# Kernel optimization log

Measured on AMD Instinct MI355X. Metric: run time of the kernel, lower is better.

The kernel has to match this reference:

```python
import jax, jax.numpy as jnp
import numpy as np

QK_DIM = 1024
V_DIM = 1024
NUM_HEADS = 16
HEAD_DIM = 64
INNER = NUM_HEADS * HEAD_DIM  # 1024
SCALE = HEAD_DIM ** -0.5


def setup_inputs() -> dict:
    key = jax.random.key(0)
    ks = jax.random.split(key, 8)
    m, nq, nkv = 4, 2048, 2048
    xq = jax.random.normal(ks[0], (m, nq, QK_DIM), dtype=jnp.float32)
    xk = jax.random.normal(ks[1], (m, nkv, QK_DIM), dtype=jnp.float32)
    xv = jax.random.normal(ks[2], (m, nkv, V_DIM), dtype=jnp.float32)
    # torch nn.Linear weights are [out, in]; y = x @ W.T
    s_qk = (QK_DIM) ** -0.5
    s_in = (INNER) ** -0.5
    Wq = jax.random.uniform(ks[3], (INNER, QK_DIM), jnp.float32, -s_qk, s_qk)
    Wk = jax.random.uniform(ks[4], (INNER, QK_DIM), jnp.float32, -s_qk, s_qk)
    Wv = jax.random.uniform(ks[5], (INNER, V_DIM), jnp.float32, -s_qk, s_qk)
    Wo = jax.random.uniform(ks[6], (V_DIM, INNER), jnp.float32, -s_in, s_in)
    bo = jax.random.uniform(ks[7], (V_DIM,), jnp.float32, -s_in, s_in)
    return {"xq": xq, "xk": xk, "xv": xv, "Wq": Wq, "Wk": Wk, "Wv": Wv, "Wo": Wo, "bo": bo}


def reference(xq, xk, xv, Wq, Wk, Wv, Wo, bo):
    m, nq, _ = xq.shape
    nkv = xk.shape[1]
    # projections (no bias), split heads: b n (h d) -> b h n d
    q = (xq @ Wq.T).reshape(m, nq, NUM_HEADS, HEAD_DIM).transpose(0, 2, 1, 3)
    k = (xk @ Wk.T).reshape(m, nkv, NUM_HEADS, HEAD_DIM).transpose(0, 2, 1, 3)
    v = (xv @ Wv.T).reshape(m, nkv, NUM_HEADS, HEAD_DIM).transpose(0, 2, 1, 3)
    dots = jnp.einsum("bhqd,bhkd->bhqk", q, k) * SCALE  # [m,h,nq,nkv]
    attn = jax.nn.softmax(dots, axis=-1)
    out = jnp.einsum("bhqk,bhkd->bhqd", attn, v)
    out = out.transpose(0, 2, 1, 3).reshape(m, nq, INNER)  # b h n d -> b n (h d)
    return out @ Wo.T + bo  # to_out Linear (dropout p=0 -> identity)
```

## Files before the change

### kernel.cpp

```cpp
#include <hip/hip_runtime.h>

typedef unsigned short u16;
using bf16x8 = __attribute__((ext_vector_type(8))) __bf16;
using f32x4  = __attribute__((ext_vector_type(4))) float;

#define QSCALE 0.18033688011f

#define EXP2F(x) __builtin_amdgcn_exp2f(x)
#define SCHED_FENCE() __builtin_amdgcn_sched_barrier(0)

__device__ __forceinline__ u16 f2bf(float f) {
  union { float f; unsigned int u; } x; x.f = f;
  unsigned int r = x.u + 0x7FFFu + ((x.u >> 16) & 1u);
  return (u16)(r >> 16);
}

__device__ __forceinline__ bf16x8 ld8(const u16* p) {
  return *reinterpret_cast<const bf16x8*>(p);
}

__device__ __forceinline__ void gload16(const void* g, void* l) {
  __builtin_amdgcn_global_load_lds(
      (const __attribute__((address_space(1))) unsigned int*)g,
      (__attribute__((address_space(3))) unsigned int*)l, 16, 0, 0);
}

__device__ __forceinline__ void cast8(const float* __restrict__ src, u16* __restrict__ dst,
                                      size_t i8) {
  const float4 v0 = reinterpret_cast<const float4*>(src)[i8 * 2];
  const float4 v1 = reinterpret_cast<const float4*>(src)[i8 * 2 + 1];
  ushort4 o0, o1;
  o0.x = f2bf(v0.x); o0.y = f2bf(v0.y); o0.z = f2bf(v0.z); o0.w = f2bf(v0.w);
  o1.x = f2bf(v1.x); o1.y = f2bf(v1.y); o1.z = f2bf(v1.z); o1.w = f2bf(v1.w);
  uint4 o;
  o.x = (unsigned)o0.x | ((unsigned)o0.y << 16);
  o.y = (unsigned)o0.z | ((unsigned)o0.w << 16);
  o.z = (unsigned)o1.x | ((unsigned)o1.y << 16);
  o.w = (unsigned)o1.z | ((unsigned)o1.w << 16);
  reinterpret_cast<uint4*>(dst)[i8] = o;
}

__global__ void cast3_f32_to_bf16(const float* __restrict__ a, const float* __restrict__ b,
                                  const float* __restrict__ c, u16* __restrict__ out, int n8) {
  const int y = blockIdx.y;
  const float* src = (y == 0) ? a : (y == 1) ? b : c;
  u16* dst = out + (size_t)y * n8 * 8;
  const int stride = gridDim.x * 256;
  for (size_t i = blockIdx.x * 256 + threadIdx.x; i < (size_t)n8; i += stride)
    cast8(src, dst, i);
}

__global__ void cast4_f32_to_bf16(const float* __restrict__ a, const float* __restrict__ b,
                                  const float* __restrict__ c, const float* __restrict__ d,
                                  u16* __restrict__ out, int n8) {
  const int y = blockIdx.y;
  const float* src = (y == 0) ? a : (y == 1) ? b : (y == 2) ? c : d;
  u16* dst = out + (size_t)y * n8 * 8;
  const int stride = gridDim.x * 256;
  for (size_t i = blockIdx.x * 256 + threadIdx.x; i < (size_t)n8; i += stride)
    cast8(src, dst, i);
}

#define GEMM64_BODY(A_, B_)                                                          \
  __shared__ alignas(16) u16 lds_a[2][128 * 64];                                     \
  __shared__ alignas(16) u16 lds_b[2][128 * 64];                                     \
  const int t = threadIdx.x;                                                         \
  const int w = t >> 6, lane = t & 63;                                               \
  const int wr = w >> 1, wc = w & 1;                                                 \
  f32x4 acc[4][4];                                                                   \
  _Pragma("unroll") for (int i = 0; i < 4; ++i)                                      \
    _Pragma("unroll") for (int j = 0; j < 4; ++j) acc[i][j] = {0.f, 0.f, 0.f, 0.f};  \
  const int b_r = t >> 3;                                                            \
  const int b_c = ((t & 7) ^ (b_r & 7)) * 8;                                         \
  const u16* gaa = A_ + (row0 + b_r) * 1024 + b_c;                                   \
  const u16* gbb = B_ + (col0 + b_r) * 1024 + b_c;                                   \
  const int fr = lane & 15;                                                          \
  const int flh = lane >> 4;                                                         \
  const int fx7 = fr & 7;                                                            \
  _Pragma("unroll") for (int s = 0; s < 4; ++s) {                                    \
    gload16(gaa + (size_t)(32 * s) * 1024, &lds_a[0][s * 2048 + w * 512]);           \
    gload16(gbb + (size_t)(32 * s) * 1024, &lds_b[0][s * 2048 + w * 512]);           \
  }                                                                                  \
  for (int it = 0; it < 16; ++it) {                                                  \
    const int cur = it & 1;                                                          \
    asm volatile("s_waitcnt vmcnt(0)" ::: "memory");                                 \
    SCHED_FENCE();                                                                   \
    __syncthreads();                                                                 \
    SCHED_FENCE();                                                                   \
    if (it != 15) {                                                                  \
      const int nk = (it + 1) * 64;                                                  \
      _Pragma("unroll") for (int s = 0; s < 4; ++s) {                                \
        gload16(gaa + (size_t)(32 * s) * 1024 + nk, &lds_a[cur ^ 1][s * 2048 + w * 512]); \
        gload16(gbb + (size_t)(32 * s) * 1024 + nk, &lds_b[cur ^ 1][s * 2048 + w * 512]); \
      }                                                                              \
    }                                                                                \
    SCHED_FENCE();                                                                   \
    _Pragma("unroll") for (int ks2 = 0; ks2 < 2; ++ks2) {                            \
      bf16x8 af[4], bfr[4];                                                          \
      const int gch = ks2 * 4 + flh;                                                 \
      _Pragma("unroll") for (int i = 0; i < 4; ++i)                                  \
        af[i] = ld8(&lds_a[cur][(wr * 64 + i * 16 + fr) * 64 + ((gch ^ fx7) * 8)]);  \
      _Pragma("unroll") for (int j = 0; j < 4; ++j)                                  \
        bfr[j] = ld8(&lds_b[cur][(wc * 64 + j * 16 + fr) * 64 + ((gch ^ fx7) * 8)]); \
      _Pragma("unroll") for (int i = 0; i < 4; ++i)                                  \
        _Pragma("unroll") for (int j = 0; j < 4; ++j)                                \
          acc[i][j] = __builtin_amdgcn_mfma_f32_16x16x32_bf16(af[i], bfr[j], acc[i][j], 0, 0, 0); \
    }                                                                                \
  }                                                                                  \
  const int er = (lane >> 4) * 4, ec = lane & 15;

__global__ __launch_bounds__(256)
void gemm_qkv(const u16* __restrict__ Aall, const u16* __restrict__ Ball,
              u16* __restrict__ Call) {
  const int g = (blockIdx.x & 7) * 192 + (blockIdx.x >> 3);
  const int bx = g & 7, by = (g >> 3) & 63, z = g >> 9;
  const u16* A = Aall + (size_t)z * 8192 * 1024;
  const u16* B = Ball + (size_t)z * 1024 * 1024;
  u16* C = Call + (size_t)z * 8192 * 1024;
  const size_t row0 = (size_t)by * 128;
  const size_t col0 = (size_t)bx * 128;

  GEMM64_BODY(A, B)

#pragma unroll
  for (int i = 0; i < 4; ++i)
#pragma unroll
    for (int j = 0; j < 4; ++j) {
      const size_t row = row0 + wr * 64 + i * 16 + er;
      const size_t col = col0 + wc * 64 + j * 16 + ec;
      if (z == 0) {
#pragma unroll
        for (int r = 0; r < 4; ++r)
          C[(row + r) * 1024 + col] = f2bf(acc[i][j][r] * QSCALE);
      } else if (z == 1) {
#pragma unroll
        for (int r = 0; r < 4; ++r) {
          const size_t n = row + r;
          const size_t colswz = (col & ~(size_t)63) |
                                ((col & 63) ^ (((n & 7) << 3)));
          C[n * 1024 + colswz] = f2bf(acc[i][j][r]);
        }
      } else {
        ushort4 o4;
        o4.x = f2bf(acc[i][j][0]); o4.y = f2bf(acc[i][j][1]);
        o4.z = f2bf(acc[i][j][2]); o4.w = f2bf(acc[i][j][3]);
        const size_t nloc = row & 2047;
        const size_t d = col & 63;
        size_t pos = (nloc & ~(size_t)31) | (((nloc >> 2) & 3) << 3) |
                     (((nloc >> 4) & 1) << 2) | (nloc & 3);
        pos ^= (d & 7) << 3;
        const size_t idx = (((row >> 11) * 16 + (col >> 6)) * 64 + d) * 2048 + pos;
        *reinterpret_cast<ushort4*>(&C[idx]) = o4;
      }
    }
}

__global__ __launch_bounds__(256)
void gemm_out(const u16* __restrict__ A, const u16* __restrict__ B,
              float* __restrict__ Cf, const float* __restrict__ bias) {
  const int g = (blockIdx.x & 7) * 64 + (blockIdx.x >> 3);
  const int bx = g & 7, by = g >> 3;
  const size_t row0 = (size_t)by * 128;
  const size_t col0 = (size_t)bx * 128;

  GEMM64_BODY(A, B)

#pragma unroll
  for (int i = 0; i < 4; ++i)
#pragma unroll
    for (int j = 0; j < 4; ++j) {
      const size_t row = row0 + wr * 64 + i * 16 + er;
      const size_t col = col0 + wc * 64 + j * 16 + ec;
#pragma unroll
      for (int r = 0; r < 4; ++r)
        Cf[(row + r) * 1024 + col] = acc[i][j][r] + bias[col];
    }
}

__global__ __launch_bounds__(512)
void flash_attn(const u16* __restrict__ Q, const u16* __restrict__ Km,
                const u16* __restrict__ Vt, u16* __restrict__ O) {
  const int o_blk = (blockIdx.x & 7) * 64 + (blockIdx.x >> 3);
  const int qt = o_blk & 7, h = (o_blk >> 3) & 15, b = o_blk >> 7;
  const int t = threadIdx.x;
  const int w = t >> 6, lane = t & 63;
  const int l16 = lane & 15, lh = lane >> 4;

  __shared__ alignas(16) u16 kt_lds[2][64][64];
  __shared__ alignas(16) u16 vt_lds[2][64][64];

  const size_t base_qk = ((size_t)b * 2048) * 1024 + (size_t)h * 64;
  const size_t base_vt = ((size_t)(b * 16 + h)) * 64 * 2048;

  bf16x8 qf[2][2];
#pragma unroll
  for (int g = 0; g < 2; ++g) {
    const size_t qrow = (size_t)qt * 256 + (w * 2 + g) * 16 + l16;
    const u16* qp = Q + base_qk + qrow * 1024 + lh * 8;
    qf[g][0] = ld8(qp);
    qf[g][1] = ld8(qp + 32);
  }

  bf16x8 vones;
#pragma unroll
  for (int i = 0; i < 8; ++i) vones[i] = (__bf16)1.0f;

  f32x4 o_acc[2][4];
  f32x4 o_sum[2];
#pragma unroll
  for (int g = 0; g < 2; ++g) {
#pragma unroll
    for (int j = 0; j < 4; ++j) o_acc[g][j] = {0.f, 0.f, 0.f, 0.f};
    o_sum[g] = {0.f, 0.f, 0.f, 0.f};
  }

  const int srow = t >> 3;
  const int schk = (t & 7) * 8;
  const u16* kg = Km + base_qk + (size_t)srow * 1024 + schk;
  const u16* vg = Vt + base_vt + (size_t)srow * 2048 + schk;
  u16* kl0 = &kt_lds[0][0][0] + w * 512;
  u16* kl1 = &kt_lds[1][0][0] + w * 512;
  u16* vl0 = &vt_lds[0][0][0] + w * 512;
  u16* vl1 = &vt_lds[1][0][0] + w * 512;

  gload16(kg, kl0);
  gload16(vg, vl0);

  const int xo = (l16 & 7) << 3;

  for (int it = 0; it < 32; ++it) {
    const int cur = it & 1;
    asm volatile("s_waitcnt vmcnt(0)" ::: "memory");
    SCHED_FENCE();
    __syncthreads();
    SCHED_FENCE();

    if (it != 31) {
      const int nkv = (it + 1) * 64;
      gload16(kg + (size_t)nkv * 1024, cur ? kl0 : kl1);
      gload16(vg + nkv, cur ? vl0 : vl1);
    }
    SCHED_FENCE();

    f32x4 s[2][4];
#pragma unroll
    for (int g = 0; g < 2; ++g)
#pragma unroll
      for (int j = 0; j < 4; ++j) s[g][j] = {0.f, 0.f, 0.f, 0.f};
    __builtin_amdgcn_s_setprio(1);
#pragma unroll
    for (int j = 0; j < 4; ++j)
#pragma unroll
      for (int ks = 0; ks < 2; ++ks) {
        bf16x8 kf = ld8(&kt_lds[cur][j * 16 + l16][(ks * 32 + lh * 8) ^ xo]);
        s[0][j] = __builtin_amdgcn_mfma_f32_16x16x32_bf16(kf, qf[0][ks], s[0][j], 0, 0, 0);
        s[1][j] = __builtin_amdgcn_mfma_f32_16x16x32_bf16(kf, qf[1][ks], s[1][j], 0, 0, 0);
      }
    __builtin_amdgcn_s_setprio(0);

    bf16x8 pa[2][2];
#pragma unroll
    for (int g = 0; g < 2; ++g)
#pragma unroll
      for (int j = 0; j < 4; ++j)
#pragma unroll
        for (int r = 0; r < 4; ++r)
          s[g][j][r] = EXP2F(s[g][j][r]);
#pragma unroll
    for (int g = 0; g < 2; ++g)
#pragma unroll
      for (int c = 0; c < 2; ++c)
#pragma unroll
        for (int i = 0; i < 8; ++i)
          pa[g][c][i] = (__bf16)s[g][2 * c + (i >> 2)][i & 3];

    __builtin_amdgcn_s_setprio(1);
#pragma unroll
    for (int c = 0; c < 2; ++c) {
      o_sum[0] = __builtin_amdgcn_mfma_f32_16x16x32_bf16(pa[0][c], vones, o_sum[0], 0, 0, 0);
      o_sum[1] = __builtin_amdgcn_mfma_f32_16x16x32_bf16(pa[1][c], vones, o_sum[1], 0, 0, 0);
#pragma unroll
      for (int jd = 0; jd < 4; ++jd) {
        bf16x8 vf = ld8(&vt_lds[cur][jd * 16 + l16][(c * 32 + lh * 8) ^ xo]);
        o_acc[0][jd] = __builtin_amdgcn_mfma_f32_16x16x32_bf16(pa[0][c], vf, o_acc[0][jd], 0, 0, 0);
        o_acc[1][jd] = __builtin_amdgcn_mfma_f32_16x16x32_bf16(pa[1][c], vf, o_acc[1][jd], 0, 0, 0);
      }
    }
    __builtin_amdgcn_s_setprio(0);
  }

#pragma unroll
  for (int g = 0; g < 2; ++g) {
    float linv[4];
#pragma unroll
    for (int r = 0; r < 4; ++r) linv[r] = 1.0f / o_sum[g][r];
    const size_t orow0 = (size_t)b * 2048 + (size_t)qt * 256 + (w * 2 + g) * 16;
#pragma unroll
    for (int jd = 0; jd < 4; ++jd) {
      const int col = h * 64 + jd * 16 + l16;
#pragma unroll
      for (int r = 0; r < 4; ++r)
        O[(orow0 + lh * 4 + r) * 1024 + col] = f2bf(o_acc[g][jd][r] * linv[r]);
    }
  }
}

extern "C" void kernel_launch(void* const* d_in, const int* in_sizes, int n_in,
                              void* d_out, int out_size, void* d_ws, size_t ws_size,
                              hipStream_t stream) {
  const float* xq = (const float*)d_in[0];
  const float* xk = (const float*)d_in[1];
  const float* xv = (const float*)d_in[2];
  const float* Wq = (const float*)d_in[3];
  const float* Wk = (const float*)d_in[4];
  const float* Wv = (const float*)d_in[5];
  const float* Wo = (const float*)d_in[6];
  const float* bo = (const float*)d_in[7];
  float* out = (float*)d_out;

  const size_t X = (size_t)8192 * 1024;
  const size_t W = (size_t)1024 * 1024;

  u16* p = (u16*)d_ws;
  u16* x_bf  = p; p += 3 * X;
  u16* w_bf  = p; p += 4 * W;
  u16* qkv   = p; p += 3 * X;
  u16* attn_bf = x_bf;

  dim3 blk(256);
  cast3_f32_to_bf16<<<dim3(2048, 3), blk, 0, stream>>>(xq, xk, xv, x_bf, (int)(X / 8));
  cast4_f32_to_bf16<<<dim3(512, 4), blk, 0, stream>>>(Wq, Wk, Wv, Wo, w_bf, (int)(W / 8));

  gemm_qkv<<<dim3(1536), blk, 0, stream>>>(x_bf, w_bf, qkv);

  flash_attn<<<dim3(512), dim3(512), 0, stream>>>(qkv, qkv + X, qkv + 2 * X, attn_bf);

  gemm_out<<<dim3(512), blk, 0, stream>>>(attn_bf, w_bf + 3 * W, out, bo);
}
```

Before: 178.2 us.

## Merge input/weight casts into one launch and use K=32 double-buffered QKV GEMM

Fuses the two f32-to-bf16 cast kernels into a single 7-slice launch, so one kernel launch and its tail are removed. The QKV projection GEMM moves to a new main loop with K-tile 32, double-buffered LDS, a new XOR swizzle, and the next tile's global-to-LDS load issued before the MFMAs on the current one. Halving the LDS footprint may raise occupancy, but it doubles the number of barrier and waitcnt iterations per output tile. Weight-cast blocks in the merged kernel use a grid sized for the activations, so many of them sit idle.

```diff
diff --git a/kernel.cpp b/kernel.cpp
--- a/kernel.cpp
+++ b/kernel.cpp
@@ -40,26 +40,66 @@
   reinterpret_cast<uint4*>(dst)[i8] = o;
 }
 
-__global__ void cast3_f32_to_bf16(const float* __restrict__ a, const float* __restrict__ b,
-                                  const float* __restrict__ c, u16* __restrict__ out, int n8) {
+__global__ void cast7_f32_to_bf16(const float* __restrict__ xq, const float* __restrict__ xk,
+                                  const float* __restrict__ xv, const float* __restrict__ wq,
+                                  const float* __restrict__ wk, const float* __restrict__ wv,
+                                  const float* __restrict__ wo, u16* __restrict__ out,
+                                  int xn8, int wn8) {
   const int y = blockIdx.y;
-  const float* src = (y == 0) ? a : (y == 1) ? b : c;
-  u16* dst = out + (size_t)y * n8 * 8;
-  const int stride = gridDim.x * 256;
-  for (size_t i = blockIdx.x * 256 + threadIdx.x; i < (size_t)n8; i += stride)
+  const float* src = (y == 0) ? xq : (y == 1) ? xk : (y == 2) ? xv
+                   : (y == 3) ? wq : (y == 4) ? wk : (y == 5) ? wv : wo;
+  const size_t n8 = (y < 3) ? (size_t)xn8 : (size_t)wn8;
+  u16* dst = out + ((y < 3) ? (size_t)y * xn8 : (size_t)3 * xn8 + (size_t)(y - 3) * wn8) * 8;
+  const size_t stride = (size_t)gridDim.x * 256;
+  for (size_t i = (size_t)blockIdx.x * 256 + threadIdx.x; i < n8; i += stride)
     cast8(src, dst, i);
 }
 
-__global__ void cast4_f32_to_bf16(const float* __restrict__ a, const float* __restrict__ b,
-                                  const float* __restrict__ c, const float* __restrict__ d,
-                                  u16* __restrict__ out, int n8) {
-  const int y = blockIdx.y;
-  const float* src = (y == 0) ? a : (y == 1) ? b : (y == 2) ? c : d;
-  u16* dst = out + (size_t)y * n8 * 8;
-  const int stride = gridDim.x * 256;
-  for (size_t i = blockIdx.x * 256 + threadIdx.x; i < (size_t)n8; i += stride)
-    cast8(src, dst, i);
-}
+#define GEMM32DB_BODY(A_, B_)                                                        \
+  __shared__ alignas(16) u16 lds_a[2][128 * 32];                                     \
+  __shared__ alignas(16) u16 lds_b[2][128 * 32];                                     \
+  const int t = threadIdx.x;                                                         \
+  const int w = t >> 6, lane = t & 63;                                               \
+  const int wr = w >> 1, wc = w & 1;                                                 \
+  f32x4 acc[4][4];                                                                   \
+  _Pragma("unroll") for (int i = 0; i < 4; ++i)                                      \
+    _Pragma("unroll") for (int j = 0; j < 4; ++j) acc[i][j] = {0.f, 0.f, 0.f, 0.f};  \
+  const int r2 = t >> 2;                                                             \
+  const int sg = (r2 + (r2 >> 2)) & 3;                                               \
+  const int c2 = ((t & 3) ^ sg) * 8;                                                 \
+  const u16* gaa = A_ + (row0 + r2) * 1024 + c2;                                     \
+  const u16* gbb = B_ + (col0 + r2) * 1024 + c2;                                     \
+  const int fr = lane & 15;                                                          \
+  const int flh = lane >> 4;                                                         \
+  const int fko = ((flh ^ ((fr + (fr >> 2)) & 3)) * 8);                              \
+  _Pragma("unroll") for (int s = 0; s < 2; ++s) {                                    \
+    gload16(gaa + (size_t)(64 * s) * 1024, &lds_a[0][s * 2048 + w * 512]);           \
+    gload16(gbb + (size_t)(64 * s) * 1024, &lds_b[0][s * 2048 + w * 512]);           \
+  }                                                                                  \
+  for (int it = 0; it < 32; ++it) {                                                  \
+    const int cur = it & 1;                                                          \
+    asm volatile("s_waitcnt vmcnt(0)" ::: "memory");                                 \
+    SCHED_FENCE();                                                                   \
+    __syncthreads();                                                                 \
+    SCHED_FENCE();                                                                   \
+    if (it != 31) {                                                                  \
+      const int nk = (it + 1) * 32;                                                  \
+      _Pragma("unroll") for (int s = 0; s < 2; ++s) {                                \
+        gload16(gaa + (size_t)(64 * s) * 1024 + nk, &lds_a[cur ^ 1][s * 2048 + w * 512]); \
+        gload16(gbb + (size_t)(64 * s) * 1024 + nk, &lds_b[cur ^ 1][s * 2048 + w * 512]); \
+      }                                                                              \
+    }                                                                                \
+    SCHED_FENCE();                                                                   \
+    bf16x8 af[4], bfr[4];                                                            \
+    _Pragma("unroll") for (int i = 0; i < 4; ++i)                                    \
+      af[i] = ld8(&lds_a[cur][(wr * 64 + i * 16 + fr) * 32 + fko]);                  \
+    _Pragma("unroll") for (int j = 0; j < 4; ++j)                                    \
+      bfr[j] = ld8(&lds_b[cur][(wc * 64 + j * 16 + fr) * 32 + fko]);                 \
+    _Pragma("unroll") for (int i = 0; i < 4; ++i)                                    \
+      _Pragma("unroll") for (int j = 0; j < 4; ++j)                                  \
+        acc[i][j] = __builtin_amdgcn_mfma_f32_16x16x32_bf16(af[i], bfr[j], acc[i][j], 0, 0, 0); \
+  }                                                                                  \
+  const int er = (lane >> 4) * 4, ec = lane & 15;
 
 #define GEMM64_BODY(A_, B_)                                                          \
   __shared__ alignas(16) u16 lds_a[2][128 * 64];                                     \
@@ -120,7 +160,7 @@
   const size_t row0 = (size_t)by * 128;
   const size_t col0 = (size_t)bx * 128;
 
-  GEMM64_BODY(A, B)
+  GEMM32DB_BODY(A, B)
 
 #pragma unroll
   for (int i = 0; i < 4; ++i)
@@ -328,8 +368,8 @@
   u16* attn_bf = x_bf;
 
   dim3 blk(256);
-  cast3_f32_to_bf16<<<dim3(2048, 3), blk, 0, stream>>>(xq, xk, xv, x_bf, (int)(X / 8));
-  cast4_f32_to_bf16<<<dim3(512, 4), blk, 0, stream>>>(Wq, Wk, Wv, Wo, w_bf, (int)(W / 8));
+  cast7_f32_to_bf16<<<dim3(2048, 7), blk, 0, stream>>>(xq, xk, xv, Wq, Wk, Wv, Wo,
+                                                       x_bf, (int)(X / 8), (int)(W / 8));
 
   gemm_qkv<<<dim3(1536), blk, 0, stream>>>(x_bf, w_bf, qkv);
 
```

After: 189.2 us. +6.2%, slower.
